# Performance work log

Hardware: AMD Instinct MI355X
Metric: run time of the kernel (lower is better)

Reference implementation:

```python
import jax, jax.numpy as jnp
import numpy as np

B, N_LR, N_HR, D, NH, L, K = 16, 256, 512, 512, 8, 4, 4
FF = 4 * D

def _ln(x, g, b):
    m = jnp.mean(x, -1, keepdims=True)
    v = jnp.var(x, -1, keepdims=True)
    return (x - m) * jax.lax.rsqrt(v + 1e-5) * g + b

def _gelu(x):
    return jax.nn.gelu(x, approximate=False)  # torch nn.GELU default = exact

def _attn(x, qkvW, qkvb, projW, projb, bias):
    b, n, d = x.shape
    hd = d // NH
    qkv = (x @ qkvW + qkvb).reshape(b, n, 3, NH, hd).transpose(2, 0, 3, 1, 4)
    q, k, v = qkv[0], qkv[1], qkv[2]
    a = jnp.einsum('bhnd,bhmd->bhnm', q, k) * (hd ** -0.5)
    if bias is not None:
        a = a + bias
    a = jax.nn.softmax(a, axis=-1)
    o = jnp.einsum('bhnm,bhmd->bhnd', a, v).transpose(0, 2, 1, 3).reshape(b, n, d)
    return o @ projW + projb

def _ffn(x, W1, b1, W2, b2):
    return _gelu(x @ W1 + b1) @ W2 + b2

def setup_inputs() -> dict:
    key = jax.random.key(0)
    ks = iter(jax.random.split(key, 64))
    def rn(shape, s=0.02):
        return jax.random.normal(next(ks), shape, jnp.float32) * s
    inp = {}
    A = rn((B, N_LR, N_LR), 1.0)
    A = 0.5 * (A + A.transpose(0, 2, 1))  # symmetric weighted adjacency
    inp['A_lr'] = A
    inp['X_lr'] = A  # node features = adjacency rows, as in the original model
    inp['ip_W'] = rn((N_LR, D)); inp['ip_b'] = jnp.zeros(D)
    inp['ip_g'] = jnp.ones(D); inp['ip_bt'] = jnp.zeros(D)
    inp['e_n1g'] = jnp.ones((L, D)); inp['e_n1b'] = jnp.zeros((L, D))
    inp['e_qkvW'] = rn((L, D, 3 * D)); inp['e_qkvb'] = jnp.zeros((L, 3 * D))
    inp['e_projW'] = rn((L, D, D)); inp['e_projb'] = jnp.zeros((L, D))
    inp['e_ebW'] = rn((L, NH), 1.0); inp['e_ebs'] = jnp.full((L,), 0.1)
    inp['e_n2g'] = jnp.ones((L, D)); inp['e_n2b'] = jnp.zeros((L, D))
    inp['e_f1W'] = rn((L, D, FF)); inp['e_f1b'] = jnp.zeros((L, FF))
    inp['e_f2W'] = rn((L, FF, D)); inp['e_f2b'] = jnp.zeros((L, D))
    inp['encn_g'] = jnp.ones(D); inp['encn_b'] = jnp.zeros(D)
    inp['up1W'] = rn((N_LR, N_HR)); inp['up1b'] = jnp.zeros(N_HR)
    inp['up2W'] = rn((N_HR, N_HR)); inp['up2b'] = jnp.zeros(N_HR)
    inp['r_n1g'] = jnp.ones(D); inp['r_n1b'] = jnp.zeros(D)
    inp['r_qkvW'] = rn((D, 3 * D)); inp['r_qkvb'] = jnp.zeros(3 * D)
    inp['r_projW'] = rn((D, D)); inp['r_projb'] = jnp.zeros(D)
    inp['r_n2g'] = jnp.ones(D); inp['r_n2b'] = jnp.zeros(D)
    inp['r_f1W'] = rn((D, FF)); inp['r_f1b'] = jnp.zeros(FF)
    inp['r_f2W'] = rn((FF, D)); inp['r_f2b'] = jnp.zeros(D)
    inp['hrn_g'] = jnp.ones(D); inp['hrn_b'] = jnp.zeros(D)
    inp['dec_W'] = rn((K, D, D)); inp['dec_b'] = jnp.full((1,), 3.0)
    return inp

def reference(A_lr, X_lr, ip_W, ip_b, ip_g, ip_bt, e_n1g, e_n1b, e_qkvW, e_qkvb, e_projW, e_projb, e_ebW, e_ebs, e_n2g, e_n2b, e_f1W, e_f1b, e_f2W, e_f2b, encn_g, encn_b, up1W, up1b, up2W, up2b, r_n1g, r_n1b, r_qkvW, r_qkvb, r_projW, r_projb, r_n2g, r_n2b, r_f1W, r_f1b, r_f2W, r_f2b, hrn_g, hrn_b, dec_W, dec_b):
    # input_proj: Linear -> LayerNorm -> GELU (dropout is identity in eval)
    H = _gelu(_ln(X_lr @ ip_W + ip_b, ip_g, ip_bt))  # (B, n_lr, D)
    # encoder: pre-norm blocks with additive per-head edge bias in softmax
    for l in range(L):
        bias = e_ebs[l] * A_lr[:, None, :, :] * e_ebW[l][None, :, None, None]  # (B,NH,N,N)
        H = H + _attn(_ln(H, e_n1g[l], e_n1b[l]), e_qkvW[l], e_qkvb[l], e_projW[l], e_projb[l], bias)
        H = H + _ffn(_ln(H, e_n2g[l], e_n2b[l]), e_f1W[l], e_f1b[l], e_f2W[l], e_f2b[l])
    H = _ln(H, encn_g, encn_b)
    # upsample n_lr -> n_hr along node axis (applied on transposed H)
    Ht = H.transpose(0, 2, 1)                      # (B, D, n_lr)
    Ht = _gelu(Ht @ up1W + up1b) @ up2W + up2b     # (B, D, n_hr)
    H = Ht.transpose(0, 2, 1)                      # (B, n_hr, D)
    # HR refinement: standard pre-norm self-attention block
    H = H + _attn(_ln(H, r_n1g, r_n1b), r_qkvW, r_qkvb, r_projW, r_projb, None)
    H = H + _ffn(_ln(H, r_n2g, r_n2b), r_f1W, r_f1b, r_f2W, r_f2b)
    H = _ln(H, hrn_g, hrn_b)
    # bilinear multi-head decoder: mean_k H W_k H^T, symmetrized
    A_pred = jnp.einsum('bnd,kde,bme->bnm', H, dec_W, H) / K
    A_pred = 0.5 * (A_pred + A_pred.transpose(0, 2, 1))
    iu, ju = np.triu_indices(N_HR, k=1)
    pred = A_pred[:, iu, ju]                        # (B, n_hr*(n_hr-1)/2)
    return jax.nn.softplus(pred + dec_b[0])
```

## Files before the change

kernel.cpp:

```cpp
#include <hip/hip_runtime.h>
#include <hip/hip_bf16.h>
#include <math.h>

#define DEV __device__ __forceinline__

typedef __attribute__((ext_vector_type(8))) short bf16x8;
typedef __attribute__((ext_vector_type(4))) float f32x4;

DEV float gelu_f(float x) {
  float u = 1.5957691f * x * (1.0f + 0.044715f * x * x);
  return x / (1.0f + __expf(-u));
}

DEV float block_reduce(float v, bool is_sum, float* red) {
#pragma unroll
  for (int off = 32; off > 0; off >>= 1) {
    float o = __shfl_down(v, off, 64);
    v = is_sum ? (v + o) : fmaxf(v, o);
  }
  __syncthreads();
  if ((threadIdx.x & 63) == 0) red[threadIdx.x >> 6] = v;
  __syncthreads();
  return is_sum ? (red[0] + red[1] + red[2] + red[3])
                : fmaxf(fmaxf(red[0], red[1]), fmaxf(red[2], red[3]));
}

DEV short bf16s(float x) {
  __hip_bfloat16 v = __float2bfloat16(x);
  return *reinterpret_cast<short*>(&v);
}

DEV void async16(void* lds, const void* g) {
  __builtin_amdgcn_global_load_lds(
      (const __attribute__((address_space(1))) unsigned int*)g,
      (__attribute__((address_space(3))) unsigned int*)lds, 16, 0, 0);
}

__global__ __launch_bounds__(256) void conv2_kernel(
    const float* __restrict__ X1, __hip_bfloat16* __restrict__ Y1,
    const float* __restrict__ X2, __hip_bfloat16* __restrict__ Y2, int n) {
  int i = blockIdx.x * 256 + threadIdx.x;
  if (i < n) {
    Y1[i] = __float2bfloat16(X1[i]);
    Y2[i] = __float2bfloat16(X2[i]);
  }
}

struct CvArgs {
  const float* s[11];
  __hip_bfloat16* d[11];
};

__global__ __launch_bounds__(256) void multi_tconv_kernel(CvArgs a) {
  const int Rj[11] = {256, 512, 512, 512, 2048, 256, 512, 512, 512, 512, 2048};
  const int Cj[11] = {512, 1536, 512, 2048, 512, 512, 512, 1536, 512, 2048, 512};
  const int Nj[11] = {1, 4, 4, 4, 4, 1, 1, 1, 1, 1, 1};
  __shared__ float t[32][33];
  int rem = blockIdx.x, j = 0;
  for (; j < 11; ++j) {
    int tj = (Rj[j] >> 5) * (Cj[j] >> 5) * Nj[j];
    if (rem < tj) break;
    rem -= tj;
  }
  const int R = Rj[j], C = Cj[j];
  const int perb = (R >> 5) * (C >> 5);
  const int z = rem / perb;
  const int tt = rem % perb;
  const int tc = C >> 5;
  const int r0 = (tt / tc) << 5, c0 = (tt % tc) << 5;
  const float* xb = a.s[j] + (size_t)z * R * C;
  __hip_bfloat16* yb = a.d[j] + (size_t)z * R * C;
  int tx = threadIdx.x & 31, ty = threadIdx.x >> 5;
  for (int i = ty; i < 32; i += 8) t[i][tx] = xb[(size_t)(r0 + i) * C + c0 + tx];
  __syncthreads();
  for (int i = ty; i < 32; i += 8)
    yb[(size_t)(c0 + i) * R + r0 + tx] = __float2bfloat16(t[tx][i]);
}

__global__ __launch_bounds__(256) void build_s_kernel(
    const float* __restrict__ W, __hip_bfloat16* __restrict__ S, int D, int Kk) {
  int i = blockIdx.x * 256 + threadIdx.x;
  if (i >= D * D) return;
  int d = i / D, e = i % D;
  float s = 0.f;
  for (int k = 0; k < Kk; ++k) {
    s += W[(size_t)k * D * D + i];
    s += W[(size_t)k * D * D + (size_t)e * D + d];
  }
  S[i] = __float2bfloat16(s / (2.0f * Kk));
}

__global__ __launch_bounds__(256) void mgemm_kernel(
    const __hip_bfloat16* __restrict__ A, const __hip_bfloat16* __restrict__ Bt,
    const float* __restrict__ bias, const float* __restrict__ resid,
    float* __restrict__ outf, __hip_bfloat16* __restrict__ outb,
    int M, int N, int K, int act, int mgrp) {
  __shared__ __align__(16) short As[2][64 * 64];
  __shared__ __align__(16) short Bs[2][64 * 64];
  const int tid = threadIdx.x;
  const int lane = tid & 63, wave = tid >> 6;
  const int quad = lane >> 4, l15 = lane & 15;
  const int bid = blockIdx.x;
  const int g = bid & 7, sidx = bid >> 3;
  const int mt = g * mgrp + sidx % mgrp;
  const int nt = sidx / mgrp;
  const int row0 = mt * 64, col0 = nt * 64;
  const short* Ag = (const short*)A;
  const short* Bg = (const short*)Bt;

  auto stage = [&](int bsel, int k0) {
#pragma unroll
    for (int i = 0; i < 2; ++i) {
      int c = (wave * 2 + i) * 64 + lane;
      int r = c >> 3, pp = c & 7;
      int kc = pp ^ (r & 7);
      async16(&As[bsel][(wave * 2 + i) * 512], &Ag[(size_t)(row0 + r) * K + k0 + kc * 8]);
      async16(&Bs[bsel][(wave * 2 + i) * 512], &Bg[(size_t)(col0 + r) * K + k0 + kc * 8]);
    }
  };

  f32x4 acc[4] = {};
  const int nk = K >> 6;
  stage(0, 0);
  for (int t = 0; t < nk; ++t) {
    const int cur = t & 1;
    __syncthreads();
    if (t + 1 < nk) stage(cur ^ 1, (t + 1) << 6);
#pragma unroll
    for (int kh = 0; kh < 2; ++kh) {
      const int ch = ((quad + kh * 4) ^ (l15 & 7)) * 8;
      bf16x8 af = *(const bf16x8*)&As[cur][(wave * 16 + l15) * 64 + ch];
#pragma unroll
      for (int ni = 0; ni < 4; ++ni) {
        bf16x8 bq = *(const bf16x8*)&Bs[cur][(ni * 16 + l15) * 64 + ch];
        acc[ni] = __builtin_amdgcn_mfma_f32_16x16x32_bf16(af, bq, acc[ni], 0, 0, 0);
      }
    }
  }

#pragma unroll
  for (int ni = 0; ni < 4; ++ni) {
    int cc = col0 + ni * 16 + l15;
    float bb = bias ? bias[cc] : 0.f;
#pragma unroll
    for (int r = 0; r < 4; ++r) {
      int rr = row0 + wave * 16 + quad * 4 + r;
      size_t idx = (size_t)rr * N + cc;
      float v = acc[ni][r] + bb;
      if (act) v = gelu_f(v);
      if (resid) v += resid[idx];
      if (outf) outf[idx] = v;
      if (outb) outb[idx] = __float2bfloat16(v);
    }
  }
}

__global__ __launch_bounds__(256) void qkv_gemm_kernel(
    const __hip_bfloat16* __restrict__ A, const __hip_bfloat16* __restrict__ Bt,
    const float* __restrict__ bias, __hip_bfloat16* __restrict__ qkv,
    int M, int K, int nseq, int lgn, int mgrp) {
  __shared__ __align__(16) short As[2][64 * 64];
  __shared__ __align__(16) short Bs[2][64 * 64];
  const int tid = threadIdx.x;
  const int lane = tid & 63, wave = tid >> 6;
  const int quad = lane >> 4, l15 = lane & 15;
  const int bid = blockIdx.x;
  const int g = bid & 7, sidx = bid >> 3;
  const int mt = g * mgrp + sidx % mgrp;
  const int nt = sidx / mgrp;
  const int row0 = mt * 64, col0 = nt * 64;
  const short* Ag = (const short*)A;
  const short* Bg = (const short*)Bt;

  auto stage = [&](int bsel, int k0) {
#pragma unroll
    for (int i = 0; i < 2; ++i) {
      int c = (wave * 2 + i) * 64 + lane;
      int r = c >> 3, pp = c & 7;
      int kc = pp ^ (r & 7);
      async16(&As[bsel][(wave * 2 + i) * 512], &Ag[(size_t)(row0 + r) * K + k0 + kc * 8]);
      async16(&Bs[bsel][(wave * 2 + i) * 512], &Bg[(size_t)(col0 + r) * K + k0 + kc * 8]);
    }
  };

  f32x4 acc[4] = {};
  const int nk = K >> 6;
  stage(0, 0);
  for (int t = 0; t < nk; ++t) {
    const int cur = t & 1;
    __syncthreads();
    if (t + 1 < nk) stage(cur ^ 1, (t + 1) << 6);
#pragma unroll
    for (int kh = 0; kh < 2; ++kh) {
      const int ch = ((quad + kh * 4) ^ (l15 & 7)) * 8;
      bf16x8 af = *(const bf16x8*)&As[cur][(wave * 16 + l15) * 64 + ch];
#pragma unroll
      for (int ni = 0; ni < 4; ++ni) {
        bf16x8 bq = *(const bf16x8*)&Bs[cur][(ni * 16 + l15) * 64 + ch];
        acc[ni] = __builtin_amdgcn_mfma_f32_16x16x32_bf16(af, bq, acc[ni], 0, 0, 0);
      }
    }
  }

  const size_t PART = (size_t)M * 512;
#pragma unroll
  for (int ni = 0; ni < 4; ++ni) {
    int cc = col0 + ni * 16 + l15;
    float bb = bias ? bias[cc] : 0.f;
    int which = cc >> 9;
    int h = (cc >> 6) & 7;
    int d = cc & 63;
#pragma unroll
    for (int r = 0; r < 4; ++r) {
      int rr = row0 + wave * 16 + quad * 4 + r;
      int b = rr >> lgn;
      int nn = rr & (nseq - 1);
      float v = acc[ni][r] + bb;
      size_t dst;
      if (which == 2) {
        dst = 2 * PART + (((size_t)b * 8 + h) * 64 + d) * nseq + nn;
      } else {
        dst = (size_t)which * PART + (((size_t)b * 8 + h) * nseq + nn) * 64 + d;
      }
      qkv[dst] = __float2bfloat16(v);
    }
  }
}

__global__ __launch_bounds__(256) void fattn_kernel(
    const __hip_bfloat16* __restrict__ Qh, const __hip_bfloat16* __restrict__ Kh,
    const __hip_bfloat16* __restrict__ Vt, __hip_bfloat16* __restrict__ O,
    const __hip_bfloat16* __restrict__ Abias, const float* __restrict__ ebW,
    const float* __restrict__ ebs, int N, int lgq) {
  __shared__ __align__(16) short Ks[2][64 * 64];
  __shared__ __align__(16) short Vs[2][64 * 64];
  __shared__ __align__(16) short Ps[4][16][72];
  const int bid = blockIdx.x;
  const int g = bid & 7, s = bid >> 3;
  const int bloc = s >> (lgq + 3);
  const int rem = s & ((8 << lgq) - 1);
  const int h = rem >> lgq;
  const int qt = rem & ((1 << lgq) - 1);
  const int b = g * 2 + bloc;
  const int tid = threadIdx.x, lane = tid & 63, wave = tid >> 6;
  const int quad = lane >> 4, l15 = lane & 15;
  const size_t hb = (size_t)b * 8 + h;
  const short* Qg = (const short*)Qh + hb * N * 64;
  const short* Kg = (const short*)Kh + hb * N * 64;
  const short* Vg = (const short*)Vt + hb * 64 * N;
  const float scale = 0.125f;
  const bool hasb = (Abias != nullptr);
  const float bscale = hasb ? ebs[0] * ebW[h] : 0.f;
  const int qrow_w = qt * 64 + wave * 16;

  auto stageKV = [&](int bsel, int k0) {
#pragma unroll
    for (int i = 0; i < 2; ++i) {
      int c = (wave * 2 + i) * 64 + lane;
      int r = c >> 3, pp = c & 7;
      int kc = pp ^ (r & 7);
      async16(&Ks[bsel][(wave * 2 + i) * 512], &Kg[(size_t)(k0 + r) * 64 + kc * 8]);
      async16(&Vs[bsel][(wave * 2 + i) * 512], &Vg[(size_t)r * N + k0 + kc * 8]);
    }
  };

  bf16x8 qf[2];
  qf[0] = *(const bf16x8*)&Qg[(size_t)(qrow_w + l15) * 64 + quad * 8];
  qf[1] = *(const bf16x8*)&Qg[(size_t)(qrow_w + l15) * 64 + quad * 8 + 32];

  float l_r[4] = {0.f, 0.f, 0.f, 0.f};
  f32x4 oacc[4] = {};

  const int ntl = N >> 6;
  stageKV(0, 0);
  for (int t = 0; t < ntl; ++t) {
    const int cur = t & 1;
    const int k0 = t << 6;
    __syncthreads();
    if (t + 1 < ntl) stageKV(cur ^ 1, (t + 1) << 6);

    f32x4 sv[4] = {};
#pragma unroll
    for (int kh = 0; kh < 2; ++kh) {
      const int ch = ((quad + kh * 4) ^ (l15 & 7)) * 8;
#pragma unroll
      for (int ni = 0; ni < 4; ++ni) {
        bf16x8 kf = *(const bf16x8*)&Ks[cur][(ni * 16 + l15) * 64 + ch];
        sv[ni] = __builtin_amdgcn_mfma_f32_16x16x32_bf16(qf[kh], kf, sv[ni], 0, 0, 0);
      }
    }
    if (hasb) {
#pragma unroll
      for (int ni = 0; ni < 4; ++ni)
#pragma unroll
        for (int r = 0; r < 4; ++r) {
          int qq = qrow_w + quad * 4 + r;
          int kk = k0 + ni * 16 + l15;
          float ab = __bfloat162float(Abias[((size_t)b * N + qq) * N + kk]);
          sv[ni][r] = sv[ni][r] * scale + bscale * ab;
        }
    } else {
#pragma unroll
      for (int ni = 0; ni < 4; ++ni)
#pragma unroll
        for (int r = 0; r < 4; ++r) sv[ni][r] *= scale;
    }

#pragma unroll
    for (int ni = 0; ni < 4; ++ni)
#pragma unroll
      for (int r = 0; r < 4; ++r) {
        float p = __expf(sv[ni][r]);
        sv[ni][r] = p;
        l_r[r] += p;
      }

#pragma unroll
    for (int ni = 0; ni < 4; ++ni)
#pragma unroll
      for (int r = 0; r < 4; ++r)
        Ps[wave][quad * 4 + r][ni * 16 + l15] = bf16s(sv[ni][r]);

    bf16x8 pf0 = *(const bf16x8*)&Ps[wave][l15][quad * 8];
    bf16x8 pf1 = *(const bf16x8*)&Ps[wave][l15][quad * 8 + 32];
#pragma unroll
    for (int kh = 0; kh < 2; ++kh) {
      const int ch = ((quad + kh * 4) ^ (l15 & 7)) * 8;
#pragma unroll
      for (int ni = 0; ni < 4; ++ni) {
        bf16x8 vf = *(const bf16x8*)&Vs[cur][(ni * 16 + l15) * 64 + ch];
        oacc[ni] = __builtin_amdgcn_mfma_f32_16x16x32_bf16(kh ? pf1 : pf0, vf, oacc[ni], 0, 0, 0);
      }
    }
  }

#pragma unroll
  for (int off = 1; off < 16; off <<= 1)
#pragma unroll
    for (int r = 0; r < 4; ++r) l_r[r] += __shfl_xor(l_r[r], off, 64);
  float inv[4];
#pragma unroll
  for (int r = 0; r < 4; ++r) inv[r] = 1.f / l_r[r];
#pragma unroll
  for (int ni = 0; ni < 4; ++ni)
#pragma unroll
    for (int r = 0; r < 4; ++r) {
      int nn = qrow_w + quad * 4 + r;
      int col = h * 64 + ni * 16 + l15;
      O[((size_t)b * N + nn) * 512 + col] = __float2bfloat16(oacc[ni][r] * inv[r]);
    }
}

__global__ __launch_bounds__(256) void dec_mfma_kernel(
    const __hip_bfloat16* __restrict__ Tb_, const __hip_bfloat16* __restrict__ Hb_,
    const float* __restrict__ dec_b, float* __restrict__ out) {
  const int Nn = 512, K = 512;
  __shared__ __align__(16) short As[2][64 * 64];
  __shared__ __align__(16) short Bs[2][64 * 64];
  int p = blockIdx.x;
  int bb = blockIdx.y;
  int it = 0, rem = p;
  while (rem >= 8 - it) { rem -= 8 - it; ++it; }
  int jt = it + rem;
  const int row0 = it * 64, col0 = jt * 64;
  const int tid = threadIdx.x;
  const int lane = tid & 63, wave = tid >> 6;
  const int quad = lane >> 4, l15 = lane & 15;
  const int wr = (wave >> 1) * 32, wc = (wave & 1) * 32;
  const short* Ag = (const short*)(Tb_ + (size_t)bb * Nn * K);
  const short* Bg = (const short*)(Hb_ + (size_t)bb * Nn * K);

  auto stage = [&](int bsel, int k0) {
#pragma unroll
    for (int i = 0; i < 2; ++i) {
      int c = (wave * 2 + i) * 64 + lane;
      int r = c >> 3, pp = c & 7;
      int kc = pp ^ (r & 7);
      async16(&As[bsel][(wave * 2 + i) * 512], &Ag[(size_t)(row0 + r) * K + k0 + kc * 8]);
      async16(&Bs[bsel][(wave * 2 + i) * 512], &Bg[(size_t)(col0 + r) * K + k0 + kc * 8]);
    }
  };

  f32x4 acc[2][2] = {};
  const int nk = K >> 6;
  stage(0, 0);
  for (int t = 0; t < nk; ++t) {
    const int cur = t & 1;
    __syncthreads();
    if (t + 1 < nk) stage(cur ^ 1, (t + 1) << 6);
#pragma unroll
    for (int kh = 0; kh < 2; ++kh) {
      const int ch = ((quad + kh * 4) ^ (l15 & 7)) * 8;
      bf16x8 af[2], bq[2];
#pragma unroll
      for (int mi = 0; mi < 2; ++mi)
        af[mi] = *(const bf16x8*)&As[cur][(wr + mi * 16 + l15) * 64 + ch];
#pragma unroll
      for (int ni = 0; ni < 2; ++ni)
        bq[ni] = *(const bf16x8*)&Bs[cur][(wc + ni * 16 + l15) * 64 + ch];
#pragma unroll
      for (int mi = 0; mi < 2; ++mi)
#pragma unroll
        for (int ni = 0; ni < 2; ++ni)
          acc[mi][ni] = __builtin_amdgcn_mfma_f32_16x16x32_bf16(af[mi], bq[ni], acc[mi][ni], 0, 0, 0);
    }
  }

  float db = dec_b[0];
  size_t obase = (size_t)bb * ((size_t)Nn * (Nn - 1) / 2);
#pragma unroll
  for (int mi = 0; mi < 2; ++mi) {
#pragma unroll
    for (int ni = 0; ni < 2; ++ni) {
      int j = col0 + wc + ni * 16 + l15;
#pragma unroll
      for (int r = 0; r < 4; ++r) {
        int i = row0 + wr + mi * 16 + quad * 4 + r;
        if (j > i) {
          float x = acc[mi][ni][r] + db;
          float sp = fmaxf(x, 0.f) + __logf(1.f + __expf(-fabsf(x)));
          out[obase + (size_t)i * (2 * Nn - i - 1) / 2 + (j - i - 1)] = sp;
        }
      }
    }
  }
}

__global__ __launch_bounds__(256) void ln_kernel(
    const float* __restrict__ X, float* __restrict__ outf,
    __hip_bfloat16* __restrict__ outb, const float* __restrict__ g,
    const float* __restrict__ b, int D, int do_gelu) {
  __shared__ float red[4];
  int row = blockIdx.x;
  const float* x = X + (size_t)row * D;
  float s = 0.f, s2 = 0.f;
  for (int d = threadIdx.x; d < D; d += 256) {
    float v = x[d];
    s += v;
    s2 += v * v;
  }
  s = block_reduce(s, true, red);
  s2 = block_reduce(s2, true, red);
  float mean = s / D;
  float var = s2 / D - mean * mean;
  float inv = rsqrtf(var + 1e-5f);
  for (int d = threadIdx.x; d < D; d += 256) {
    float v = (x[d] - mean) * inv * g[d] + b[d];
    if (do_gelu) v = gelu_f(v);
    if (outf) outf[(size_t)row * D + d] = v;
    if (outb) outb[(size_t)row * D + d] = __float2bfloat16(v);
  }
}

template <typename T>
__global__ __launch_bounds__(256) void transpose_kernel(
    const T* __restrict__ X, T* __restrict__ Y, int R, int C) {
  __shared__ T t[32][33];
  const T* xb = X + (size_t)blockIdx.z * R * C;
  T* yb = Y + (size_t)blockIdx.z * R * C;
  int c0 = blockIdx.x * 32, r0 = blockIdx.y * 32;
  int tx = threadIdx.x & 31, ty = threadIdx.x >> 5;
  for (int i = ty; i < 32; i += 8) t[i][tx] = xb[(size_t)(r0 + i) * C + c0 + tx];
  __syncthreads();
  for (int i = ty; i < 32; i += 8) yb[(size_t)(c0 + i) * R + r0 + tx] = t[tx][i];
}

extern "C" void kernel_launch(void* const* d_in, const int* in_sizes, int n_in,
                              void* d_out, int out_size, void* d_ws, size_t ws_size,
                              hipStream_t stream) {
  const float *A_lr = (const float*)d_in[0], *X_lr = (const float*)d_in[1],
              *ip_W = (const float*)d_in[2], *ip_b = (const float*)d_in[3],
              *ip_g = (const float*)d_in[4], *ip_bt = (const float*)d_in[5],
              *e_n1g = (const float*)d_in[6], *e_n1b = (const float*)d_in[7],
              *e_qkvW = (const float*)d_in[8], *e_qkvb = (const float*)d_in[9],
              *e_projW = (const float*)d_in[10], *e_projb = (const float*)d_in[11],
              *e_ebW = (const float*)d_in[12], *e_ebs = (const float*)d_in[13],
              *e_n2g = (const float*)d_in[14], *e_n2b = (const float*)d_in[15],
              *e_f1W = (const float*)d_in[16], *e_f1b = (const float*)d_in[17],
              *e_f2W = (const float*)d_in[18], *e_f2b = (const float*)d_in[19],
              *encn_g = (const float*)d_in[20], *encn_b = (const float*)d_in[21],
              *up1W = (const float*)d_in[22], *up1b = (const float*)d_in[23],
              *up2W = (const float*)d_in[24], *up2b = (const float*)d_in[25],
              *r_n1g = (const float*)d_in[26], *r_n1b = (const float*)d_in[27],
              *r_qkvW = (const float*)d_in[28], *r_qkvb = (const float*)d_in[29],
              *r_projW = (const float*)d_in[30], *r_projb = (const float*)d_in[31],
              *r_n2g = (const float*)d_in[32], *r_n2b = (const float*)d_in[33],
              *r_f1W = (const float*)d_in[34], *r_f1b = (const float*)d_in[35],
              *r_f2W = (const float*)d_in[36], *r_f2b = (const float*)d_in[37],
              *hrn_g = (const float*)d_in[38], *hrn_b = (const float*)d_in[39],
              *dec_W = (const float*)d_in[40], *dec_b = (const float*)d_in[41];

  const int Bb = 16, NLR = 256, NHR = 512, Dm = 512, NHh = 8, FF = 2048, Ll = 4;
  typedef __hip_bfloat16 bf;

  float* ws = (float*)d_ws;
  float* H = ws;
  float* Hf = ws + 4194304;
  bf* XNb = (bf*)(ws + 8388608);
  bf* AOb = (bf*)(ws + 10485760);
  bf* BIGb = (bf*)(ws + 12582912);
  bf* WB = (bf*)(ws + 20971520);
  bf* Xlrb = (bf*)(ws + 29229056);
  bf* Albrb = (bf*)(ws + 29753344);

  size_t o = 0;
  bf* ipWt = WB + o;   o += (size_t)512 * 256;
  bf* eqkvT = WB + o;  o += (size_t)4 * 1536 * 512;
  bf* eprojT = WB + o; o += (size_t)4 * 512 * 512;
  bf* ef1T = WB + o;   o += (size_t)4 * 2048 * 512;
  bf* ef2T = WB + o;   o += (size_t)4 * 512 * 2048;
  bf* up1T = WB + o;   o += (size_t)512 * 256;
  bf* up2T = WB + o;   o += (size_t)512 * 512;
  bf* rqkvT = WB + o;  o += (size_t)1536 * 512;
  bf* rprojT = WB + o; o += (size_t)512 * 512;
  bf* rf1T = WB + o;   o += (size_t)2048 * 512;
  bf* rf2T = WB + o;   o += (size_t)512 * 2048;
  bf* Sb = WB + o;     o += (size_t)512 * 512;

  bf* Q_e = BIGb;
  bf* K_e = BIGb + 2097152;
  bf* V_e = BIGb + 4194304;
  bf* Q_r = BIGb;
  bf* K_r = BIGb + 4194304;
  bf* V_r = BIGb + 8388608;

  CvArgs cv;
  cv.s[0] = ip_W;   cv.d[0] = ipWt;
  cv.s[1] = e_qkvW; cv.d[1] = eqkvT;
  cv.s[2] = e_projW; cv.d[2] = eprojT;
  cv.s[3] = e_f1W;  cv.d[3] = ef1T;
  cv.s[4] = e_f2W;  cv.d[4] = ef2T;
  cv.s[5] = up1W;   cv.d[5] = up1T;
  cv.s[6] = up2W;   cv.d[6] = up2T;
  cv.s[7] = r_qkvW; cv.d[7] = rqkvT;
  cv.s[8] = r_projW; cv.d[8] = rprojT;
  cv.s[9] = r_f1W;  cv.d[9] = rf1T;
  cv.s[10] = r_f2W; cv.d[10] = rf2T;
  multi_tconv_kernel<<<15872, 256, 0, stream>>>(cv);
  conv2_kernel<<<(1048576 + 255) / 256, 256, 0, stream>>>(
      X_lr, Xlrb, A_lr, Albrb, 1048576);
  build_s_kernel<<<(512 * 512 + 255) / 256, 256, 0, stream>>>(dec_W, Sb, Dm, 4);

  mgemm_kernel<<<64 * 8, 256, 0, stream>>>(
      Xlrb, ipWt, ip_b, nullptr, Hf, nullptr, Bb * NLR, Dm, NLR, 0, 8);
  ln_kernel<<<Bb * NLR, 256, 0, stream>>>(Hf, H, nullptr, ip_g, ip_bt, Dm, 1);

  for (int l = 0; l < Ll; ++l) {
    ln_kernel<<<Bb * NLR, 256, 0, stream>>>(H, nullptr, XNb, e_n1g + l * Dm, e_n1b + l * Dm, Dm, 0);
    qkv_gemm_kernel<<<64 * 24, 256, 0, stream>>>(
        XNb, eqkvT + (size_t)l * 1536 * 512, e_qkvb + l * 1536, BIGb,
        Bb * NLR, Dm, NLR, 8, 8);
    fattn_kernel<<<16 * 8 * 4, 256, 0, stream>>>(
        Q_e, K_e, V_e, AOb, Albrb, e_ebW + l * NHh, e_ebs + l, NLR, 2);
    mgemm_kernel<<<64 * 8, 256, 0, stream>>>(
        AOb, eprojT + (size_t)l * 512 * 512, e_projb + l * Dm, H,
        H, nullptr, Bb * NLR, Dm, Dm, 0, 8);
    ln_kernel<<<Bb * NLR, 256, 0, stream>>>(H, nullptr, XNb, e_n2g + l * Dm, e_n2b + l * Dm, Dm, 0);
    mgemm_kernel<<<64 * 32, 256, 0, stream>>>(
        XNb, ef1T + (size_t)l * 2048 * 512, e_f1b + l * FF, nullptr,
        nullptr, BIGb, Bb * NLR, FF, Dm, 1, 8);
    mgemm_kernel<<<64 * 8, 256, 0, stream>>>(
        BIGb, ef2T + (size_t)l * 512 * 2048, e_f2b + l * Dm, H,
        H, nullptr, Bb * NLR, Dm, FF, 0, 8);
  }

  ln_kernel<<<Bb * NLR, 256, 0, stream>>>(H, nullptr, XNb, encn_g, encn_b, Dm, 0);
  transpose_kernel<bf><<<dim3(16, 8, Bb), 256, 0, stream>>>(XNb, AOb, NLR, Dm);
  mgemm_kernel<<<128 * 8, 256, 0, stream>>>(
      AOb, up1T, up1b, nullptr, nullptr, BIGb, Bb * Dm, NHR, NLR, 1, 16);
  mgemm_kernel<<<128 * 8, 256, 0, stream>>>(
      BIGb, up2T, up2b, nullptr, Hf, nullptr, Bb * Dm, NHR, NHR, 0, 16);
  transpose_kernel<float><<<dim3(16, 16, Bb), 256, 0, stream>>>(Hf, H, Dm, NHR);

  ln_kernel<<<Bb * NHR, 256, 0, stream>>>(H, nullptr, XNb, r_n1g, r_n1b, Dm, 0);
  qkv_gemm_kernel<<<128 * 24, 256, 0, stream>>>(
      XNb, rqkvT, r_qkvb, BIGb, Bb * NHR, Dm, NHR, 9, 16);
  fattn_kernel<<<16 * 8 * 8, 256, 0, stream>>>(
      Q_r, K_r, V_r, AOb, nullptr, nullptr, nullptr, NHR, 3);
  mgemm_kernel<<<128 * 8, 256, 0, stream>>>(
      AOb, rprojT, r_projb, H, H, nullptr, Bb * NHR, Dm, Dm, 0, 16);
  ln_kernel<<<Bb * NHR, 256, 0, stream>>>(H, nullptr, XNb, r_n2g, r_n2b, Dm, 0);
  mgemm_kernel<<<128 * 32, 256, 0, stream>>>(
      XNb, rf1T, r_f1b, nullptr, nullptr, BIGb, Bb * NHR, FF, Dm, 1, 16);
  mgemm_kernel<<<128 * 8, 256, 0, stream>>>(
      BIGb, rf2T, r_f2b, H, H, nullptr, Bb * NHR, Dm, FF, 0, 16);

  ln_kernel<<<Bb * NHR, 256, 0, stream>>>(H, nullptr, XNb, hrn_g, hrn_b, Dm, 0);
  mgemm_kernel<<<128 * 8, 256, 0, stream>>>(
      XNb, Sb, nullptr, nullptr, nullptr, AOb, Bb * NHR, Dm, Dm, 0, 16);
  dec_mfma_kernel<<<dim3(36, Bb), 256, 0, stream>>>(
      AOb, XNb, dec_b, (float*)d_out);
}
```

Baseline: 877.3 us.

## Enlarge GEMM tiles to 128-row blocks with 2x2 wave layout; vectorize LayerNorm

The GEMM kernels move from 64x64 tiles, where each wave computes a 16x64 strip, to 128x(64|128) tiles, where each wave computes a 64xN sub-tile. Each wave now loads 4 A fragments and NJ B fragments per k-step and reuses them across a 4xNJ grid of MFMAs, cutting LDS and global traffic per flop. Grids and grouping factors are scaled to match. LayerNorm now handles one row per wave using float4 loads and shuffle-only reductions with no block sync, at the cost of a hardcoded D=512. The larger accumulators raise register and LDS pressure, which may lower occupancy, and the grids become smaller.

```diff
diff --git a/kernel.cpp b/kernel.cpp
--- a/kernel.cpp
+++ b/kernel.cpp
@@ -5,24 +5,12 @@
 #define DEV __device__ __forceinline__
 
 typedef __attribute__((ext_vector_type(8))) short bf16x8;
+typedef __attribute__((ext_vector_type(4))) short s16x4;
 typedef __attribute__((ext_vector_type(4))) float f32x4;
 
 DEV float gelu_f(float x) {
   float u = 1.5957691f * x * (1.0f + 0.044715f * x * x);
   return x / (1.0f + __expf(-u));
-}
-
-DEV float block_reduce(float v, bool is_sum, float* red) {
-#pragma unroll
-  for (int off = 32; off > 0; off >>= 1) {
-    float o = __shfl_down(v, off, 64);
-    v = is_sum ? (v + o) : fmaxf(v, o);
-  }
-  __syncthreads();
-  if ((threadIdx.x & 63) == 0) red[threadIdx.x >> 6] = v;
-  __syncthreads();
-  return is_sum ? (red[0] + red[1] + red[2] + red[3])
-                : fmaxf(fmaxf(red[0], red[1]), fmaxf(red[2], red[3]));
 }
 
 DEV short bf16s(float x) {
@@ -90,36 +78,44 @@
   S[i] = __float2bfloat16(s / (2.0f * Kk));
 }
 
+template <int NJ>
 __global__ __launch_bounds__(256) void mgemm_kernel(
     const __hip_bfloat16* __restrict__ A, const __hip_bfloat16* __restrict__ Bt,
     const float* __restrict__ bias, const float* __restrict__ resid,
     float* __restrict__ outf, __hip_bfloat16* __restrict__ outb,
     int M, int N, int K, int act, int mgrp) {
-  __shared__ __align__(16) short As[2][64 * 64];
-  __shared__ __align__(16) short Bs[2][64 * 64];
+  __shared__ __align__(16) short As[2][128 * 64];
+  __shared__ __align__(16) short Bs[2][NJ * 32 * 64];
   const int tid = threadIdx.x;
   const int lane = tid & 63, wave = tid >> 6;
   const int quad = lane >> 4, l15 = lane & 15;
+  const int wr = wave >> 1, wc = wave & 1;
   const int bid = blockIdx.x;
   const int g = bid & 7, sidx = bid >> 3;
   const int mt = g * mgrp + sidx % mgrp;
   const int nt = sidx / mgrp;
-  const int row0 = mt * 64, col0 = nt * 64;
+  const int row0 = mt * 128, col0 = nt * (NJ * 32);
   const short* Ag = (const short*)A;
   const short* Bg = (const short*)Bt;
 
   auto stage = [&](int bsel, int k0) {
 #pragma unroll
-    for (int i = 0; i < 2; ++i) {
-      int c = (wave * 2 + i) * 64 + lane;
+    for (int i = 0; i < 4; ++i) {
+      int c = i * 256 + tid;
       int r = c >> 3, pp = c & 7;
       int kc = pp ^ (r & 7);
-      async16(&As[bsel][(wave * 2 + i) * 512], &Ag[(size_t)(row0 + r) * K + k0 + kc * 8]);
-      async16(&Bs[bsel][(wave * 2 + i) * 512], &Bg[(size_t)(col0 + r) * K + k0 + kc * 8]);
+      async16(&As[bsel][c * 8], &Ag[(size_t)(row0 + r) * K + k0 + kc * 8]);
+    }
+#pragma unroll
+    for (int i = 0; i < NJ; ++i) {
+      int c = i * 256 + tid;
+      int r = c >> 3, pp = c & 7;
+      int kc = pp ^ (r & 7);
+      async16(&Bs[bsel][c * 8], &Bg[(size_t)(col0 + r) * K + k0 + kc * 8]);
     }
   };
 
-  f32x4 acc[4] = {};
+  f32x4 acc[4][NJ] = {};
   const int nk = K >> 6;
   stage(0, 0);
   for (int t = 0; t < nk; ++t) {
@@ -129,28 +125,37 @@
 #pragma unroll
     for (int kh = 0; kh < 2; ++kh) {
       const int ch = ((quad + kh * 4) ^ (l15 & 7)) * 8;
-      bf16x8 af = *(const bf16x8*)&As[cur][(wave * 16 + l15) * 64 + ch];
-#pragma unroll
-      for (int ni = 0; ni < 4; ++ni) {
-        bf16x8 bq = *(const bf16x8*)&Bs[cur][(ni * 16 + l15) * 64 + ch];
-        acc[ni] = __builtin_amdgcn_mfma_f32_16x16x32_bf16(af, bq, acc[ni], 0, 0, 0);
+      bf16x8 af[4], bq[NJ];
+#pragma unroll
+      for (int mi = 0; mi < 4; ++mi)
+        af[mi] = *(const bf16x8*)&As[cur][(wr * 64 + mi * 16 + l15) * 64 + ch];
+#pragma unroll
+      for (int ni = 0; ni < NJ; ++ni)
+        bq[ni] = *(const bf16x8*)&Bs[cur][(wc * (NJ * 16) + ni * 16 + l15) * 64 + ch];
+#pragma unroll
+      for (int mi = 0; mi < 4; ++mi)
+#pragma unroll
+        for (int ni = 0; ni < NJ; ++ni)
+          acc[mi][ni] = __builtin_amdgcn_mfma_f32_16x16x32_bf16(af[mi], bq[ni], acc[mi][ni], 0, 0, 0);
+    }
+  }
+
+#pragma unroll
+  for (int ni = 0; ni < NJ; ++ni) {
+    int cc = col0 + wc * (NJ * 16) + ni * 16 + l15;
+    float bb = bias ? bias[cc] : 0.f;
+#pragma unroll
+    for (int mi = 0; mi < 4; ++mi) {
+#pragma unroll
+      for (int r = 0; r < 4; ++r) {
+        int rr = row0 + wr * 64 + mi * 16 + quad * 4 + r;
+        size_t idx = (size_t)rr * N + cc;
+        float v = acc[mi][ni][r] + bb;
+        if (act) v = gelu_f(v);
+        if (resid) v += resid[idx];
+        if (outf) outf[idx] = v;
+        if (outb) outb[idx] = __float2bfloat16(v);
       }
-    }
-  }
-
-#pragma unroll
-  for (int ni = 0; ni < 4; ++ni) {
-    int cc = col0 + ni * 16 + l15;
-    float bb = bias ? bias[cc] : 0.f;
-#pragma unroll
-    for (int r = 0; r < 4; ++r) {
-      int rr = row0 + wave * 16 + quad * 4 + r;
-      size_t idx = (size_t)rr * N + cc;
-      float v = acc[ni][r] + bb;
-      if (act) v = gelu_f(v);
-      if (resid) v += resid[idx];
-      if (outf) outf[idx] = v;
-      if (outb) outb[idx] = __float2bfloat16(v);
     }
   }
 }
@@ -159,31 +164,38 @@
     const __hip_bfloat16* __restrict__ A, const __hip_bfloat16* __restrict__ Bt,
     const float* __restrict__ bias, __hip_bfloat16* __restrict__ qkv,
     int M, int K, int nseq, int lgn, int mgrp) {
-  __shared__ __align__(16) short As[2][64 * 64];
-  __shared__ __align__(16) short Bs[2][64 * 64];
+  __shared__ __align__(16) short As[2][128 * 64];
+  __shared__ __align__(16) short Bs[2][128 * 64];
   const int tid = threadIdx.x;
   const int lane = tid & 63, wave = tid >> 6;
   const int quad = lane >> 4, l15 = lane & 15;
+  const int wr = wave >> 1, wc = wave & 1;
   const int bid = blockIdx.x;
   const int g = bid & 7, sidx = bid >> 3;
   const int mt = g * mgrp + sidx % mgrp;
   const int nt = sidx / mgrp;
-  const int row0 = mt * 64, col0 = nt * 64;
+  const int row0 = mt * 128, col0 = nt * 128;
   const short* Ag = (const short*)A;
   const short* Bg = (const short*)Bt;
 
   auto stage = [&](int bsel, int k0) {
 #pragma unroll
-    for (int i = 0; i < 2; ++i) {
-      int c = (wave * 2 + i) * 64 + lane;
+    for (int i = 0; i < 4; ++i) {
+      int c = i * 256 + tid;
       int r = c >> 3, pp = c & 7;
       int kc = pp ^ (r & 7);
-      async16(&As[bsel][(wave * 2 + i) * 512], &Ag[(size_t)(row0 + r) * K + k0 + kc * 8]);
-      async16(&Bs[bsel][(wave * 2 + i) * 512], &Bg[(size_t)(col0 + r) * K + k0 + kc * 8]);
+      async16(&As[bsel][c * 8], &Ag[(size_t)(row0 + r) * K + k0 + kc * 8]);
+    }
+#pragma unroll
+    for (int i = 0; i < 4; ++i) {
+      int c = i * 256 + tid;
+      int r = c >> 3, pp = c & 7;
+      int kc = pp ^ (r & 7);
+      async16(&Bs[bsel][c * 8], &Bg[(size_t)(col0 + r) * K + k0 + kc * 8]);
     }
   };
 
-  f32x4 acc[4] = {};
+  f32x4 acc[4][4] = {};
   const int nk = K >> 6;
   stage(0, 0);
   for (int t = 0; t < nk; ++t) {
@@ -193,36 +205,45 @@
 #pragma unroll
     for (int kh = 0; kh < 2; ++kh) {
       const int ch = ((quad + kh * 4) ^ (l15 & 7)) * 8;
-      bf16x8 af = *(const bf16x8*)&As[cur][(wave * 16 + l15) * 64 + ch];
-#pragma unroll
-      for (int ni = 0; ni < 4; ++ni) {
-        bf16x8 bq = *(const bf16x8*)&Bs[cur][(ni * 16 + l15) * 64 + ch];
-        acc[ni] = __builtin_amdgcn_mfma_f32_16x16x32_bf16(af, bq, acc[ni], 0, 0, 0);
-      }
+      bf16x8 af[4], bq[4];
+#pragma unroll
+      for (int mi = 0; mi < 4; ++mi)
+        af[mi] = *(const bf16x8*)&As[cur][(wr * 64 + mi * 16 + l15) * 64 + ch];
+#pragma unroll
+      for (int ni = 0; ni < 4; ++ni)
+        bq[ni] = *(const bf16x8*)&Bs[cur][(wc * 64 + ni * 16 + l15) * 64 + ch];
+#pragma unroll
+      for (int mi = 0; mi < 4; ++mi)
+#pragma unroll
+        for (int ni = 0; ni < 4; ++ni)
+          acc[mi][ni] = __builtin_amdgcn_mfma_f32_16x16x32_bf16(af[mi], bq[ni], acc[mi][ni], 0, 0, 0);
     }
   }
 
   const size_t PART = (size_t)M * 512;
 #pragma unroll
   for (int ni = 0; ni < 4; ++ni) {
-    int cc = col0 + ni * 16 + l15;
+    int cc = col0 + wc * 64 + ni * 16 + l15;
     float bb = bias ? bias[cc] : 0.f;
     int which = cc >> 9;
     int h = (cc >> 6) & 7;
     int d = cc & 63;
 #pragma unroll
-    for (int r = 0; r < 4; ++r) {
-      int rr = row0 + wave * 16 + quad * 4 + r;
-      int b = rr >> lgn;
-      int nn = rr & (nseq - 1);
-      float v = acc[ni][r] + bb;
-      size_t dst;
-      if (which == 2) {
-        dst = 2 * PART + (((size_t)b * 8 + h) * 64 + d) * nseq + nn;
-      } else {
-        dst = (size_t)which * PART + (((size_t)b * 8 + h) * nseq + nn) * 64 + d;
+    for (int mi = 0; mi < 4; ++mi) {
+#pragma unroll
+      for (int r = 0; r < 4; ++r) {
+        int rr = row0 + wr * 64 + mi * 16 + quad * 4 + r;
+        int b = rr >> lgn;
+        int nn = rr & (nseq - 1);
+        float v = acc[mi][ni][r] + bb;
+        size_t dst;
+        if (which == 2) {
+          dst = 2 * PART + (((size_t)b * 8 + h) * 64 + d) * nseq + nn;
+        } else {
+          dst = (size_t)which * PART + (((size_t)b * 8 + h) * nseq + nn) * 64 + d;
+        }
+        qkv[dst] = __float2bfloat16(v);
       }
-      qkv[dst] = __float2bfloat16(v);
     }
   }
 }
@@ -429,26 +450,47 @@
 __global__ __launch_bounds__(256) void ln_kernel(
     const float* __restrict__ X, float* __restrict__ outf,
     __hip_bfloat16* __restrict__ outb, const float* __restrict__ g,
-    const float* __restrict__ b, int D, int do_gelu) {
-  __shared__ float red[4];
-  int row = blockIdx.x;
-  const float* x = X + (size_t)row * D;
-  float s = 0.f, s2 = 0.f;
-  for (int d = threadIdx.x; d < D; d += 256) {
-    float v = x[d];
-    s += v;
-    s2 += v * v;
-  }
-  s = block_reduce(s, true, red);
-  s2 = block_reduce(s2, true, red);
-  float mean = s / D;
-  float var = s2 / D - mean * mean;
-  float inv = rsqrtf(var + 1e-5f);
-  for (int d = threadIdx.x; d < D; d += 256) {
-    float v = (x[d] - mean) * inv * g[d] + b[d];
-    if (do_gelu) v = gelu_f(v);
-    if (outf) outf[(size_t)row * D + d] = v;
-    if (outb) outb[(size_t)row * D + d] = __float2bfloat16(v);
+    const float* __restrict__ b, int do_gelu) {
+  const int row = blockIdx.x * 4 + (threadIdx.x >> 6);
+  const int lane = threadIdx.x & 63;
+  const float4* x = (const float4*)X + (size_t)row * 128;
+  float4 v0 = x[lane], v1 = x[lane + 64];
+  float s = v0.x + v0.y + v0.z + v0.w + v1.x + v1.y + v1.z + v1.w;
+  float s2 = v0.x * v0.x + v0.y * v0.y + v0.z * v0.z + v0.w * v0.w +
+             v1.x * v1.x + v1.y * v1.y + v1.z * v1.z + v1.w * v1.w;
+#pragma unroll
+  for (int off = 32; off; off >>= 1) {
+    s += __shfl_xor(s, off, 64);
+    s2 += __shfl_xor(s2, off, 64);
+  }
+  const float mean = s * (1.0f / 512.0f);
+  const float inv = rsqrtf(s2 * (1.0f / 512.0f) - mean * mean + 1e-5f);
+  const float4 g0 = ((const float4*)g)[lane], g1 = ((const float4*)g)[lane + 64];
+  const float4 b0 = ((const float4*)b)[lane], b1 = ((const float4*)b)[lane + 64];
+  float4 y0, y1;
+  y0.x = (v0.x - mean) * inv * g0.x + b0.x;
+  y0.y = (v0.y - mean) * inv * g0.y + b0.y;
+  y0.z = (v0.z - mean) * inv * g0.z + b0.z;
+  y0.w = (v0.w - mean) * inv * g0.w + b0.w;
+  y1.x = (v1.x - mean) * inv * g1.x + b1.x;
+  y1.y = (v1.y - mean) * inv * g1.y + b1.y;
+  y1.z = (v1.z - mean) * inv * g1.z + b1.z;
+  y1.w = (v1.w - mean) * inv * g1.w + b1.w;
+  if (do_gelu) {
+    y0.x = gelu_f(y0.x); y0.y = gelu_f(y0.y); y0.z = gelu_f(y0.z); y0.w = gelu_f(y0.w);
+    y1.x = gelu_f(y1.x); y1.y = gelu_f(y1.y); y1.z = gelu_f(y1.z); y1.w = gelu_f(y1.w);
+  }
+  if (outf) {
+    float4* of = (float4*)outf + (size_t)row * 128;
+    of[lane] = y0;
+    of[lane + 64] = y1;
+  }
+  if (outb) {
+    s16x4 p0, p1;
+    p0.x = bf16s(y0.x); p0.y = bf16s(y0.y); p0.z = bf16s(y0.z); p0.w = bf16s(y0.w);
+    p1.x = bf16s(y1.x); p1.y = bf16s(y1.y); p1.z = bf16s(y1.z); p1.w = bf16s(y1.w);
+    *(s16x4*)((short*)outb + (size_t)row * 512 + lane * 4) = p0;
+    *(s16x4*)((short*)outb + (size_t)row * 512 + 256 + lane * 4) = p1;
   }
 }
 
@@ -541,53 +583,53 @@
       X_lr, Xlrb, A_lr, Albrb, 1048576);
   build_s_kernel<<<(512 * 512 + 255) / 256, 256, 0, stream>>>(dec_W, Sb, Dm, 4);
 
-  mgemm_kernel<<<64 * 8, 256, 0, stream>>>(
-      Xlrb, ipWt, ip_b, nullptr, Hf, nullptr, Bb * NLR, Dm, NLR, 0, 8);
-  ln_kernel<<<Bb * NLR, 256, 0, stream>>>(Hf, H, nullptr, ip_g, ip_bt, Dm, 1);
+  mgemm_kernel<2><<<256, 256, 0, stream>>>(
+      Xlrb, ipWt, ip_b, nullptr, Hf, nullptr, Bb * NLR, Dm, NLR, 0, 4);
+  ln_kernel<<<Bb * NLR / 4, 256, 0, stream>>>(Hf, H, nullptr, ip_g, ip_bt, 1);
 
   for (int l = 0; l < Ll; ++l) {
-    ln_kernel<<<Bb * NLR, 256, 0, stream>>>(H, nullptr, XNb, e_n1g + l * Dm, e_n1b + l * Dm, Dm, 0);
-    qkv_gemm_kernel<<<64 * 24, 256, 0, stream>>>(
+    ln_kernel<<<Bb * NLR / 4, 256, 0, stream>>>(H, nullptr, XNb, e_n1g + l * Dm, e_n1b + l * Dm, 0);
+    qkv_gemm_kernel<<<384, 256, 0, stream>>>(
         XNb, eqkvT + (size_t)l * 1536 * 512, e_qkvb + l * 1536, BIGb,
-        Bb * NLR, Dm, NLR, 8, 8);
+        Bb * NLR, Dm, NLR, 8, 4);
     fattn_kernel<<<16 * 8 * 4, 256, 0, stream>>>(
         Q_e, K_e, V_e, AOb, Albrb, e_ebW + l * NHh, e_ebs + l, NLR, 2);
-    mgemm_kernel<<<64 * 8, 256, 0, stream>>>(
+    mgemm_kernel<2><<<256, 256, 0, stream>>>(
         AOb, eprojT + (size_t)l * 512 * 512, e_projb + l * Dm, H,
-        H, nullptr, Bb * NLR, Dm, Dm, 0, 8);
-    ln_kernel<<<Bb * NLR, 256, 0, stream>>>(H, nullptr, XNb, e_n2g + l * Dm, e_n2b + l * Dm, Dm, 0);
-    mgemm_kernel<<<64 * 32, 256, 0, stream>>>(
+        H, nullptr, Bb * NLR, Dm, Dm, 0, 4);
+    ln_kernel<<<Bb * NLR / 4, 256, 0, stream>>>(H, nullptr, XNb, e_n2g + l * Dm, e_n2b + l * Dm, 0);
+    mgemm_kernel<4><<<512, 256, 0, stream>>>(
         XNb, ef1T + (size_t)l * 2048 * 512, e_f1b + l * FF, nullptr,
-        nullptr, BIGb, Bb * NLR, FF, Dm, 1, 8);
-    mgemm_kernel<<<64 * 8, 256, 0, stream>>>(
+        nullptr, BIGb, Bb * NLR, FF, Dm, 1, 4);
+    mgemm_kernel<2><<<256, 256, 0, stream>>>(
         BIGb, ef2T + (size_t)l * 512 * 2048, e_f2b + l * Dm, H,
-        H, nullptr, Bb * NLR, Dm, FF, 0, 8);
-  }
-
-  ln_kernel<<<Bb * NLR, 256, 0, stream>>>(H, nullptr, XNb, encn_g, encn_b, Dm, 0);
+        H, nullptr, Bb * NLR, Dm, FF, 0, 4);
+  }
+
+  ln_kernel<<<Bb * NLR / 4, 256, 0, stream>>>(H, nullptr, XNb, encn_g, encn_b, 0);
   transpose_kernel<bf><<<dim3(16, 8, Bb), 256, 0, stream>>>(XNb, AOb, NLR, Dm);
-  mgemm_kernel<<<128 * 8, 256, 0, stream>>>(
-      AOb, up1T, up1b, nullptr, nullptr, BIGb, Bb * Dm, NHR, NLR, 1, 16);
-  mgemm_kernel<<<128 * 8, 256, 0, stream>>>(
-      BIGb, up2T, up2b, nullptr, Hf, nullptr, Bb * Dm, NHR, NHR, 0, 16);
+  mgemm_kernel<2><<<512, 256, 0, stream>>>(
+      AOb, up1T, up1b, nullptr, nullptr, BIGb, Bb * Dm, NHR, NLR, 1, 8);
+  mgemm_kernel<2><<<512, 256, 0, stream>>>(
+      BIGb, up2T, up2b, nullptr, Hf, nullptr, Bb * Dm, NHR, NHR, 0, 8);
   transpose_kernel<float><<<dim3(16, 16, Bb), 256, 0, stream>>>(Hf, H, Dm, NHR);
 
-  ln_kernel<<<Bb * NHR, 256, 0, stream>>>(H, nullptr, XNb, r_n1g, r_n1b, Dm, 0);
-  qkv_gemm_kernel<<<128 * 24, 256, 0, stream>>>(
-      XNb, rqkvT, r_qkvb, BIGb, Bb * NHR, Dm, NHR, 9, 16);
+  ln_kernel<<<Bb * NHR / 4, 256, 0, stream>>>(H, nullptr, XNb, r_n1g, r_n1b, 0);
+  qkv_gemm_kernel<<<768, 256, 0, stream>>>(
+      XNb, rqkvT, r_qkvb, BIGb, Bb * NHR, Dm, NHR, 9, 8);
   fattn_kernel<<<16 * 8 * 8, 256, 0, stream>>>(
       Q_r, K_r, V_r, AOb, nullptr, nullptr, nullptr, NHR, 3);
-  mgemm_kernel<<<128 * 8, 256, 0, stream>>>(
-      AOb, rprojT, r_projb, H, H, nullptr, Bb * NHR, Dm, Dm, 0, 16);
-  ln_kernel<<<Bb * NHR, 256, 0, stream>>>(H, nullptr, XNb, r_n2g, r_n2b, Dm, 0);
-  mgemm_kernel<<<128 * 32, 256, 0, stream>>>(
-      XNb, rf1T, r_f1b, nullptr, nullptr, BIGb, Bb * NHR, FF, Dm, 1, 16);
-  mgemm_kernel<<<128 * 8, 256, 0, stream>>>(
-      BIGb, rf2T, r_f2b, H, H, nullptr, Bb * NHR, Dm, FF, 0, 16);
-
-  ln_kernel<<<Bb * NHR, 256, 0, stream>>>(H, nullptr, XNb, hrn_g, hrn_b, Dm, 0);
-  mgemm_kernel<<<128 * 8, 256, 0, stream>>>(
-      XNb, Sb, nullptr, nullptr, nullptr, AOb, Bb * NHR, Dm, Dm, 0, 16);
+  mgemm_kernel<2><<<512, 256, 0, stream>>>(
+      AOb, rprojT, r_projb, H, H, nullptr, Bb * NHR, Dm, Dm, 0, 8);
+  ln_kernel<<<Bb * NHR / 4, 256, 0, stream>>>(H, nullptr, XNb, r_n2g, r_n2b, 0);
+  mgemm_kernel<4><<<1024, 256, 0, stream>>>(
+      XNb, rf1T, r_f1b, nullptr, nullptr, BIGb, Bb * NHR, FF, Dm, 1, 8);
+  mgemm_kernel<2><<<512, 256, 0, stream>>>(
+      BIGb, rf2T, r_f2b, H, H, nullptr, Bb * NHR, Dm, FF, 0, 8);
+
+  ln_kernel<<<Bb * NHR / 4, 256, 0, stream>>>(H, nullptr, XNb, hrn_g, hrn_b, 0);
+  mgemm_kernel<2><<<512, 256, 0, stream>>>(
+      XNb, Sb, nullptr, nullptr, nullptr, AOb, Bb * NHR, Dm, Dm, 0, 8);
   dec_mfma_kernel<<<dim3(36, Bb), 256, 0, stream>>>(
       AOb, XNb, dec_b, (float*)d_out);
 }
```

Result: no change. 884.5 us (+0.8%).
